# Performance work log

Hardware: AMD Instinct MI355X
Metric: run time of the kernel (lower is better)

Reference implementation:

```python
import jax, jax.numpy as jnp
import numpy as np

DIM = 3
N = DIM * DIM          # 9 digits
NUM_NODES = N * N      # 81 cells
HID = 96
EMB = 16

def sudoku_edges():
    edges = []
    for r in range(N):
        for c in range(N):
            s = set()
            for k in range(N):
                s.add(r * N + k)
                s.add(k * N + c)
            br, bc = (r // DIM) * DIM, (c // DIM) * DIM
            for dr in range(DIM):
                for dc in range(DIM):
                    s.add((br + dr) * N + (bc + dc))
            s.discard(r * N + c)
            edges.append(sorted(s))
    return np.asarray(edges, np.int32)  # (81, 20)

EDGES = jnp.asarray(sudoku_edges())

def mlp(x, params):
    # ReLU between hidden layers, no activation after the last layer
    for w, b in params[:-1]:
        x = jax.nn.relu(x @ w + b)
    w, b = params[-1]
    return x @ w + b

def setup_inputs():
    key = jax.random.key(0)
    ks = iter(jax.random.split(key, 64))
    B = 256
    def p(shape, scale=0.1):
        return jax.random.normal(next(ks), shape, jnp.float32) * scale
    inp = {}
    inp['grids'] = jax.random.randint(next(ks), (B, NUM_NODES), 0, 3)
    inp['iters'] = 8
    inp['emb'] = p((3, EMB))
    inp['in_w0'] = p((EMB, HID)); inp['in_b0'] = jnp.zeros((HID,), jnp.float32)
    inp['in_w1'] = p((HID, HID)); inp['in_b1'] = jnp.zeros((HID,), jnp.float32)
    inp['in_w2'] = p((HID, HID)); inp['in_b2'] = jnp.zeros((HID,), jnp.float32)
    inp['rel_w0'] = p((2 * HID, HID)); inp['rel_b0'] = jnp.zeros((HID,), jnp.float32)
    inp['rel_w1'] = p((HID, HID)); inp['rel_b1'] = jnp.zeros((HID,), jnp.float32)
    inp['rel_w2'] = p((HID, HID)); inp['rel_b2'] = jnp.zeros((HID,), jnp.float32)
    inp['g_w0'] = p((2 * HID, HID)); inp['g_b0'] = jnp.zeros((HID,), jnp.float32)
    inp['g_w1'] = p((HID, HID)); inp['g_b1'] = jnp.zeros((HID,), jnp.float32)
    inp['g_w2'] = p((HID, HID)); inp['g_b2'] = jnp.zeros((HID,), jnp.float32)
    inp['lstm_wih'] = p((HID, 4 * HID)); inp['lstm_whh'] = p((HID, 4 * HID))
    inp['lstm_bih'] = jnp.zeros((4 * HID,), jnp.float32)
    inp['lstm_bhh'] = jnp.zeros((4 * HID,), jnp.float32)
    inp['r_w0'] = p((HID, HID)); inp['r_b0'] = jnp.zeros((HID,), jnp.float32)
    inp['r_w1'] = p((HID, HID)); inp['r_b1'] = jnp.zeros((HID,), jnp.float32)
    inp['r_w2'] = p((HID, N)); inp['r_b2'] = jnp.zeros((N,), jnp.float32)
    inp['c0'] = p((B * NUM_NODES, HID), 1.0)  # torch.randn LSTM cell init
    return inp

def reference(grids, iters, emb, in_w0, in_b0, in_w1, in_b1, in_w2, in_b2,
              rel_w0, rel_b0, rel_w1, rel_b1, rel_w2, rel_b2,
              g_w0, g_b0, g_w1, g_b1, g_w2, g_b2,
              lstm_wih, lstm_whh, lstm_bih, lstm_bhh,
              r_w0, r_b0, r_w1, r_b1, r_w2, r_b2, c0):
    B = grids.shape[0]
    in_p = [(in_w0, in_b0), (in_w1, in_b1), (in_w2, in_b2)]
    rel_p = [(rel_w0, rel_b0), (rel_w1, rel_b1), (rel_w2, rel_b2)]
    g_p = [(g_w0, g_b0), (g_w1, g_b1), (g_w2, g_b2)]
    r_p = [(r_w0, r_b0), (r_w1, r_b1), (r_w2, r_b2)]
    X = mlp(emb[grids], in_p)                     # (B, 81, 96)
    H0 = jax.lax.stop_gradient(X)                 # X.clone().detach()
    h = H0.reshape(B * NUM_NODES, HID)
    bias = lstm_bih + lstm_bhh

    def step(carry, _):
        h, c = carry
        Hn = h.reshape(B, NUM_NODES, HID)
        nbr = Hn[:, EDGES]                        # (B, 81, 20, 96) neighbor gather
        self_f = jnp.broadcast_to(Hn[:, :, None], nbr.shape)
        msgs = mlp(jnp.concatenate([self_f, nbr], axis=-1), rel_p)
        M = msgs.sum(axis=2)                      # scatter-sum of messages
        x_in = mlp(jnp.concatenate([X, M], axis=-1), g_p).reshape(B * NUM_NODES, HID)
        gates = x_in @ lstm_wih + h @ lstm_whh + bias
        i, f, g, o = jnp.split(gates, 4, axis=-1)  # torch gate order i,f,g,o
        c2 = jax.nn.sigmoid(f) * c + jax.nn.sigmoid(i) * jnp.tanh(g)
        h2 = jax.nn.sigmoid(o) * jnp.tanh(c2)
        out = mlp(h2.reshape(B, NUM_NODES, HID), r_p)  # (B, 81, 9)
        return (h2, c2), out

    _, outputs = jax.lax.scan(step, (h, c0), None, length=iters)
    return outputs  # (iters, B, 81, 9)
```

## Files before the change

kernel.cpp:

```cpp
#include <hip/hip_runtime.h>
#include <hip/hip_bf16.h>
#include <stdint.h>

typedef __attribute__((ext_vector_type(8))) short short8v;
typedef __attribute__((ext_vector_type(4))) float float4v;

#define DEVI __device__ __forceinline__

constexpr int BATCH = 256;
constexpr int NN   = 81;
constexpr int HID  = 96;
constexpr int NOUT = 9;
constexpr int BLOCK = 512;
constexpr int LDA = 100;

constexpr int OFF_H  = 0;
constexpr int OFF_AP = 8100;
constexpr int OFF_BV = 16200;
constexpr int OFF_MS = 24300;
constexpr int OFF_XG = 32400;
constexpr int SMEM_F = 40176;

constexpr int W_REL0A = 0;
constexpr int W_REL0B = 18432;
constexpr int W_REL1  = 36864;
constexpr int W_REL2  = 55296;
constexpr int W_G0B   = 73728;
constexpr int W_G1    = 92160;
constexpr int W_G2    = 110592;
constexpr int W_IH    = 129024;
constexpr int W_HH    = 202752;
constexpr int W_R0    = 276480;
constexpr int W_R1    = 294912;
constexpr int W_R2    = 313344;
constexpr int W_IN1   = 316416;
constexpr int W_IN2   = 334848;
constexpr int W_G0A   = 353280;

DEVI float sigm(float x)  { return 1.f / (1.f + __expf(-x)); }
DEVI float tanh_(float x) { return 1.f - 2.f / (__expf(2.f * x) + 1.f); }

DEVI short bfhi(float x) { union { float f; unsigned u; } v; v.f = x; return (short)(v.u >> 16); }
DEVI float fromBits(short s) { union { unsigned u; float f; } v; v.u = ((unsigned)(unsigned short)s) << 16; return v.f; }
DEVI short bfrne(float x) {
  union { float f; unsigned u; } v; v.f = x;
  unsigned r = v.u + 0x7fffu + ((v.u >> 16) & 1u);
  return (short)(r >> 16);
}
DEVI void split1(float x, short& h, short& l) { h = bfhi(x); l = bfrne(x - fromBits(h)); }

DEVI void packFrag(const float* p, short8v& v) {
  const float4 a = *reinterpret_cast<const float4*>(p);
  const float4 b = *reinterpret_cast<const float4*>(p + 4);
  v[0] = bfrne(a.x); v[1] = bfrne(a.y); v[2] = bfrne(a.z); v[3] = bfrne(a.w);
  v[4] = bfrne(b.x); v[5] = bfrne(b.y); v[6] = bfrne(b.z); v[7] = bfrne(b.w);
}
DEVI void packFragPair(const float* ap, const float* bp, short8v& v) {
  const float4 a0 = *reinterpret_cast<const float4*>(ap);
  const float4 a1 = *reinterpret_cast<const float4*>(ap + 4);
  const float4 b0 = *reinterpret_cast<const float4*>(bp);
  const float4 b1 = *reinterpret_cast<const float4*>(bp + 4);
  v[0] = bfrne(fmaxf(a0.x + b0.x, 0.f)); v[1] = bfrne(fmaxf(a0.y + b0.y, 0.f));
  v[2] = bfrne(fmaxf(a0.z + b0.z, 0.f)); v[3] = bfrne(fmaxf(a0.w + b0.w, 0.f));
  v[4] = bfrne(fmaxf(a1.x + b1.x, 0.f)); v[5] = bfrne(fmaxf(a1.y + b1.y, 0.f));
  v[6] = bfrne(fmaxf(a1.z + b1.z, 0.f)); v[7] = bfrne(fmaxf(a1.w + b1.w, 0.f));
}

DEVI float4v mfma2(short8v a, short8v bh, short8v bl, float4v acc) {
  acc = __builtin_amdgcn_mfma_f32_16x16x32_bf16(a, bh, acc, 0, 0, 0);
  acc = __builtin_amdgcn_mfma_f32_16x16x32_bf16(a, bl, acc, 0, 0, 0);
  return acc;
}

DEVI int nbr_of(int n, int e) {
  const int r = n / 9, c = n - 9 * r;
  if (e < 8)  { int cc = c + 1 + e;  if (cc >= 9) cc -= 9; return r * 9 + cc; }
  if (e < 16) { int rr = r + e - 7;  if (rr >= 9) rr -= 9; return rr * 9 + c; }
  const int q = e - 16, dr = 1 + (q >> 1), dc = 1 + (q & 1);
  const int rm = r % 3, cm = c % 3;
  int rr = r - rm + rm + dr; rr -= (rm + dr >= 3) ? 3 : 0;
  int cc = c - cm + cm + dc; cc -= (cm + dc >= 3) ? 3 : 0;
  return rr * 9 + cc;
}

__global__ __launch_bounds__(64)
void pack_kernel(const float* rel_w0, const float* rel_w1, const float* rel_w2,
                 const float* g_w0, const float* g_w1, const float* g_w2,
                 const float* wih, const float* whh,
                 const float* r_w0, const float* r_w1, const float* r_w2,
                 const float* in_w1, const float* in_w2, short* ws)
{
  const int lane = threadIdx.x;
  const int blk = blockIdx.x;
  const int starts[16] = {0,18,36,54,72,90,108,126,198,270,288,306,309,327,345,363};
  int mi = 0;
  while (blk >= starts[mi + 1]) ++mi;
  const int tt = blk - starts[mi];
  const int ntile = starts[mi + 1] - starts[mi];
  const float* src; int C = 96, row0 = 0, off;
  switch (mi) {
    case 0:  src = rel_w0; off = W_REL0A; break;
    case 1:  src = rel_w0; row0 = 96; off = W_REL0B; break;
    case 2:  src = rel_w1; off = W_REL1; break;
    case 3:  src = rel_w2; off = W_REL2; break;
    case 4:  src = g_w0; row0 = 96; off = W_G0B; break;
    case 5:  src = g_w1; off = W_G1; break;
    case 6:  src = g_w2; off = W_G2; break;
    case 7:  src = wih; C = 384; off = W_IH; break;
    case 8:  src = whh; C = 384; off = W_HH; break;
    case 9:  src = r_w0; off = W_R0; break;
    case 10: src = r_w1; off = W_R1; break;
    case 11: src = r_w2; C = 9; off = W_R2; break;
    case 12: src = in_w1; off = W_IN1; break;
    case 13: src = in_w2; off = W_IN2; break;
    default: src = g_w0; off = W_G0A; break;
  }
  const int kt = tt % 3, ct = tt / 3;
  const int q = lane >> 4, r = lane & 15;
  const int c = ct * 16 + r;
  short* hd = ws + off + tt * 512 + lane * 8;
  short* ld = hd + ntile * 512;
  #pragma unroll
  for (int j = 0; j < 8; ++j) {
    const int k = row0 + kt * 32 + q * 8 + j;
    float w = (c < C) ? src[k * C + c] : 0.f;
    short h, l; split1(w, h, l);
    hd[j] = h; ld[j] = l;
  }
}

DEVI void stage96(float* sm, int aOff, const short* WS, int wOff, int wTiles, int CT,
                  const float* bias, float bscale, bool relu, bool xgAdd,
                  float* dst, int dstLD, int wave, int lane)
{
  const int rl = lane & 15, q = lane >> 4;
  const int plane = wTiles * 512;
  #pragma unroll 1
  for (int t = wave; t < 3 * CT; t += 8) {
    const int rtp = t % 3, ct = t / 3;
    short8v a2[2][3];
    #pragma unroll
    for (int sub = 0; sub < 2; ++sub) {
      const int row = rtp * 32 + sub * 16 + rl;
      const float* ap = &sm[aOff + row * LDA + q * 8];
      #pragma unroll
      for (int kt = 0; kt < 3; ++kt) packFrag(ap + kt * 32, a2[sub][kt]);
    }
    float4v acc0 = {0.f, 0.f, 0.f, 0.f}, acc1 = {0.f, 0.f, 0.f, 0.f};
    #pragma unroll
    for (int kt = 0; kt < 3; ++kt) {
      const short* bp = WS + wOff + (ct * 3 + kt) * 512 + lane * 8;
      const short8v bh = *reinterpret_cast<const short8v*>(bp);
      const short8v bl = *reinterpret_cast<const short8v*>(bp + plane);
      acc0 = mfma2(a2[0][kt], bh, bl, acc0);
      acc1 = mfma2(a2[1][kt], bh, bl, acc1);
    }
    const int col = ct * 16 + rl;
    #pragma unroll
    for (int sub = 0; sub < 2; ++sub) {
      #pragma unroll
      for (int j = 0; j < 4; ++j) {
        const int row = rtp * 32 + sub * 16 + q * 4 + j;
        if (row < NN) {
          float v = sub ? acc1[j] : acc0[j];
          if (bias)  v += bias[col] * bscale;
          if (xgAdd) v += sm[OFF_XG + row * 96 + col];
          if (relu)  v = fmaxf(v, 0.f);
          dst[row * dstLD + col] = v;
        }
      }
    }
  }
}

__global__ __launch_bounds__(BLOCK) __attribute__((amdgpu_waves_per_eu(1, 2)))
void rrn_kernel(const int* __restrict__ grids, const int* __restrict__ itersp,
                const float* __restrict__ emb, const float* __restrict__ in_w0,
                const float* __restrict__ in_b0, const float* __restrict__ in_b1,
                const float* __restrict__ in_b2,
                const float* __restrict__ rel_b0, const float* __restrict__ rel_b1,
                const float* __restrict__ rel_b2,
                const float* __restrict__ g_b0, const float* __restrict__ g_b1,
                const float* __restrict__ g_b2,
                const float* __restrict__ bih, const float* __restrict__ bhh,
                const float* __restrict__ r_b0, const float* __restrict__ r_b1,
                const float* __restrict__ r_b2,
                const float* __restrict__ c0, const short* __restrict__ WS,
                float* __restrict__ out)
{
  __shared__ float sm[SMEM_F];
  const int b = blockIdx.x, tid = threadIdx.x;
  const int wave = tid >> 6, lane = tid & 63;
  const int rl = lane & 15, q = lane >> 4;
  const int iters = itersp[0];

  float creg[6][4];
  #pragma unroll
  for (int rt = 0; rt < 6; ++rt)
    #pragma unroll
    for (int j = 0; j < 4; ++j) creg[rt][j] = 0.f;
  if (wave < 6) {
    #pragma unroll
    for (int rt = 0; rt < 6; ++rt) {
      #pragma unroll
      for (int j = 0; j < 4; ++j) {
        const int n = rt * 16 + q * 4 + j, col = wave * 16 + rl;
        creg[rt][j] = (n < NN) ? c0[(size_t)b * NN * HID + n * HID + col] : 0.f;
      }
    }
  }

  for (int t = tid; t < NN * HID; t += BLOCK) {
    const int n = t / HID, col = t - n * HID;
    const int g = grids[b * NN + n];
    float acc = in_b0[col];
    #pragma unroll
    for (int k = 0; k < 16; ++k) acc += emb[g * 16 + k] * in_w0[k * HID + col];
    sm[OFF_AP + n * LDA + col] = fmaxf(acc, 0.f);
  }
  __syncthreads();
  stage96(sm, OFF_AP, WS, W_IN1, 18, 6, in_b1, 1.f, true,  false, &sm[OFF_BV], LDA, wave, lane);
  __syncthreads();
  stage96(sm, OFF_BV, WS, W_IN2, 18, 6, in_b2, 1.f, false, false, &sm[OFF_H],  LDA, wave, lane);
  __syncthreads();
  stage96(sm, OFF_H,  WS, W_G0A, 18, 6, g_b0,  1.f, false, false, &sm[OFF_XG], 96,  wave, lane);
  __syncthreads();

  for (int it = 0; it < iters; ++it) {
    for (int i = tid; i < 8100; i += BLOCK) sm[OFF_MS + i] = 0.f;
    stage96(sm, OFF_H, WS, W_REL0A, 18, 6, rel_b0, 1.f, false, false, &sm[OFF_AP], LDA, wave, lane);
    stage96(sm, OFF_H, WS, W_REL0B, 18, 6, nullptr, 0.f, false, false, &sm[OFF_BV], LDA, wave, lane);
    __syncthreads();

    #pragma unroll 1
    for (int g2 = wave; g2 < 51; g2 += 8) {
      short8v a2[2][3];
      #pragma unroll
      for (int sub = 0; sub < 2; ++sub) {
        const int row = g2 * 32 + sub * 16 + rl;
        if (row < 1620) {
          const int n = row / 20, e = row - 20 * n, m = nbr_of(n, e);
          const float* ap = &sm[OFF_AP + n * LDA + q * 8];
          const float* bp = &sm[OFF_BV + m * LDA + q * 8];
          #pragma unroll
          for (int kt = 0; kt < 3; ++kt)
            packFragPair(ap + kt * 32, bp + kt * 32, a2[sub][kt]);
        } else {
          const short8v z = {0,0,0,0,0,0,0,0};
          #pragma unroll
          for (int kt = 0; kt < 3; ++kt) a2[sub][kt] = z;
        }
      }
      #pragma unroll 1
      for (int ct = 0; ct < 6; ++ct) {
        const float rb1c = rel_b1[ct * 16 + rl];
        float4v acc0 = {0,0,0,0}, acc1 = {0,0,0,0};
        #pragma unroll
        for (int kt = 0; kt < 3; ++kt) {
          const short* bp = WS + W_REL1 + (ct * 3 + kt) * 512 + lane * 8;
          const short8v bh = *reinterpret_cast<const short8v*>(bp);
          const short8v bl = *reinterpret_cast<const short8v*>(bp + 18 * 512);
          acc0 = mfma2(a2[0][kt], bh, bl, acc0);
          acc1 = mfma2(a2[1][kt], bh, bl, acc1);
        }
        const int col = ct * 16 + rl;
        #pragma unroll
        for (int sub = 0; sub < 2; ++sub) {
          const int r0 = g2 * 32 + sub * 16 + q * 4;
          if (r0 < 1620) {
            const int node = r0 / 20;
            const float4v a = sub ? acc1 : acc0;
            const float s = fmaxf(a[0] + rb1c, 0.f) + fmaxf(a[1] + rb1c, 0.f)
                          + fmaxf(a[2] + rb1c, 0.f) + fmaxf(a[3] + rb1c, 0.f);
            atomicAdd(&sm[OFF_MS + node * LDA + col], s);
          }
        }
        __builtin_amdgcn_sched_barrier(0);
      }
    }
    __syncthreads();

    stage96(sm, OFF_MS, WS, W_REL2, 18, 6, rel_b2, 20.f, false, false, &sm[OFF_AP], LDA, wave, lane);
    __syncthreads();
    stage96(sm, OFF_AP, WS, W_G0B, 18, 6, nullptr, 0.f, true, true,  &sm[OFF_BV], LDA, wave, lane);
    __syncthreads();
    stage96(sm, OFF_BV, WS, W_G1, 18, 6, g_b1, 1.f, true,  false, &sm[OFF_AP], LDA, wave, lane);
    __syncthreads();
    stage96(sm, OFF_AP, WS, W_G2, 18, 6, g_b2, 1.f, false, false, &sm[OFF_BV], LDA, wave, lane);
    __syncthreads();

    if (wave < 6) {
      const int colh = wave * 16 + rl;
      #pragma unroll
      for (int rt = 0; rt < 6; ++rt) {
        const int row = rt * 16 + rl;
        short8v af[6];
        #pragma unroll
        for (int kt = 0; kt < 3; ++kt)
          packFrag(&sm[OFF_BV + row * LDA + kt * 32 + q * 8], af[kt]);
        #pragma unroll
        for (int kt = 3; kt < 6; ++kt)
          packFrag(&sm[OFF_H + row * LDA + (kt - 3) * 32 + q * 8], af[kt]);
        float4v ga[4];
        #pragma unroll
        for (int gate = 0; gate < 4; ++gate) {
          const int ct = gate * 6 + wave;
          float4v acc = {0.f, 0.f, 0.f, 0.f};
          #pragma unroll
          for (int kt = 0; kt < 3; ++kt) {
            const short* bp = WS + W_IH + (ct * 3 + kt) * 512 + lane * 8;
            acc = mfma2(af[kt], *reinterpret_cast<const short8v*>(bp),
                        *reinterpret_cast<const short8v*>(bp + 72 * 512), acc);
          }
          __builtin_amdgcn_sched_barrier(0);
          #pragma unroll
          for (int kt = 3; kt < 6; ++kt) {
            const short* bp = WS + W_HH + (ct * 3 + kt - 3) * 512 + lane * 8;
            acc = mfma2(af[kt], *reinterpret_cast<const short8v*>(bp),
                        *reinterpret_cast<const short8v*>(bp + 72 * 512), acc);
          }
          ga[gate] = acc;
          __builtin_amdgcn_sched_barrier(0);
        }
        #pragma unroll
        for (int j = 0; j < 4; ++j) {
          const int n = rt * 16 + q * 4 + j;
          const float gi = ga[0][j] + bih[colh]       + bhh[colh];
          const float gf = ga[1][j] + bih[96 + colh]  + bhh[96 + colh];
          const float gg = ga[2][j] + bih[192 + colh] + bhh[192 + colh];
          const float go = ga[3][j] + bih[288 + colh] + bhh[288 + colh];
          const float c2 = sigm(gf) * creg[rt][j] + sigm(gi) * tanh_(gg);
          creg[rt][j] = c2;
          if (n < NN) sm[OFF_AP + n * LDA + colh] = sigm(go) * tanh_(c2);
        }
      }
    }
    __syncthreads();
    for (int i = tid; i < 8100; i += BLOCK) sm[OFF_H + i] = sm[OFF_AP + i];
    __syncthreads();

    stage96(sm, OFF_H,  WS, W_R0, 18, 6, r_b0, 1.f, true, false, &sm[OFF_AP], LDA, wave, lane);
    __syncthreads();
    stage96(sm, OFF_AP, WS, W_R1, 18, 6, r_b1, 1.f, true, false, &sm[OFF_BV], LDA, wave, lane);
    __syncthreads();
    if (wave < 3) {
      const int rtp = wave;
      short8v a2[2][3];
      #pragma unroll
      for (int sub = 0; sub < 2; ++sub) {
        const int row = rtp * 32 + sub * 16 + rl;
        #pragma unroll
        for (int kt = 0; kt < 3; ++kt)
          packFrag(&sm[OFF_BV + row * LDA + kt * 32 + q * 8], a2[sub][kt]);
      }
      float4v a0 = {0,0,0,0}, a1 = {0,0,0,0};
      #pragma unroll
      for (int kt = 0; kt < 3; ++kt) {
        const short* bp = WS + W_R2 + kt * 512 + lane * 8;
        const short8v bh = *reinterpret_cast<const short8v*>(bp);
        const short8v bl = *reinterpret_cast<const short8v*>(bp + 3 * 512);
        a0 = mfma2(a2[0][kt], bh, bl, a0);
        a1 = mfma2(a2[1][kt], bh, bl, a1);
      }
      if (rl < NOUT) {
        float* op = out + ((size_t)it * BATCH + b) * NN * NOUT;
        #pragma unroll
        for (int sub = 0; sub < 2; ++sub)
          #pragma unroll
          for (int j = 0; j < 4; ++j) {
            const int row = rtp * 32 + sub * 16 + q * 4 + j;
            if (row < NN) op[row * NOUT + rl] = (sub ? a1[j] : a0[j]) + r_b2[rl];
          }
      }
    }
    __syncthreads();
  }
}

extern "C" void kernel_launch(void* const* d_in, const int* in_sizes, int n_in,
                              void* d_out, int out_size, void* d_ws, size_t ws_size,
                              hipStream_t stream) {
  (void)in_sizes; (void)n_in; (void)out_size; (void)ws_size;
  const int* grids = (const int*)d_in[0];
  const int* iters = (const int*)d_in[1];
  const float *emb = (const float*)d_in[2],
    *in_w0 = (const float*)d_in[3],  *in_b0 = (const float*)d_in[4],
    *in_b1 = (const float*)d_in[6],  *in_b2 = (const float*)d_in[8],
    *rel_w0 = (const float*)d_in[9],  *rel_b0 = (const float*)d_in[10],
    *rel_w1 = (const float*)d_in[11], *rel_b1 = (const float*)d_in[12],
    *rel_w2 = (const float*)d_in[13], *rel_b2 = (const float*)d_in[14],
    *g_w0 = (const float*)d_in[15], *g_b0 = (const float*)d_in[16],
    *g_w1 = (const float*)d_in[17], *g_b1 = (const float*)d_in[18],
    *g_w2 = (const float*)d_in[19], *g_b2 = (const float*)d_in[20],
    *wih = (const float*)d_in[21], *whh = (const float*)d_in[22],
    *bih = (const float*)d_in[23], *bhh = (const float*)d_in[24],
    *r_w0 = (const float*)d_in[25], *r_b0 = (const float*)d_in[26],
    *r_w1 = (const float*)d_in[27], *r_b1 = (const float*)d_in[28],
    *r_w2 = (const float*)d_in[29], *r_b2 = (const float*)d_in[30],
    *c0 = (const float*)d_in[31];
  short* ws = (short*)d_ws;
  pack_kernel<<<dim3(363), dim3(64), 0, stream>>>(
      rel_w0, rel_w1, rel_w2, g_w0, g_w1, g_w2, wih, whh,
      r_w0, r_w1, r_w2, (const float*)d_in[5], (const float*)d_in[7], ws);
  rrn_kernel<<<dim3(BATCH), dim3(BLOCK), 0, stream>>>(
      grids, iters, emb, in_w0, in_b0, in_b1, in_b2,
      rel_b0, rel_b1, rel_b2, g_b0, g_b1, g_b2,
      bih, bhh, r_b0, r_b1, r_b2, c0, (const short*)ws, (float*)d_out);
}
```

Measured before the change: 919.7 us.

## Store intermediate activations as bf16 in LDS and double-buffer hidden state

The dense MLP stages now read and write their intermediate activations as bf16 in shared memory with padded stride 104. MFMA A-fragments become a single vector load instead of an fp32 read followed by packing. The hidden state is ping-ponged between two bf16 buffers, which removes the per-iteration copy loop and one barrier. This cuts LDS traffic and conversion work per stage. In exchange, more intermediates are rounded to bf16 before storage, which may slightly change numerics.

```diff
diff --git a/kernel.cpp b/kernel.cpp
--- a/kernel.cpp
+++ b/kernel.cpp
@@ -13,13 +13,15 @@
 constexpr int NOUT = 9;
 constexpr int BLOCK = 512;
 constexpr int LDA = 100;
-
-constexpr int OFF_H  = 0;
-constexpr int OFF_AP = 8100;
-constexpr int OFF_BV = 16200;
-constexpr int OFF_MS = 24300;
-constexpr int OFF_XG = 32400;
-constexpr int SMEM_F = 40176;
+constexpr int LDB = 104;
+
+constexpr int OFF_XG = 0;
+constexpr int OFF_H0 = 7776;
+constexpr int OFF_H1 = 11988;
+constexpr int OFF_MS = 16200;
+constexpr int OFF_AP = 24300;
+constexpr int OFF_BV = 32400;
+constexpr int SMEM_F = 40500;
 
 constexpr int W_REL0A = 0;
 constexpr int W_REL0B = 18432;
@@ -129,22 +131,33 @@
   }
 }
 
-DEVI void stage96(float* sm, int aOff, const short* WS, int wOff, int wTiles, int CT,
-                  const float* bias, float bscale, bool relu, bool xgAdd,
-                  float* dst, int dstLD, int wave, int lane)
+template<bool ABF, bool OBF, bool RELU, bool XGADD>
+DEVI void stage96(float* sm, int aOff, const short* WS, int wOff, int wTiles,
+                  const float* bias, float bscale, int dOff, int dstLDf,
+                  int wave, int lane)
 {
   const int rl = lane & 15, q = lane >> 4;
   const int plane = wTiles * 512;
+  const short* asb = reinterpret_cast<const short*>(sm + aOff);
+  short* dsb = reinterpret_cast<short*>(sm + dOff);
+  float* dsf = sm + dOff;
   #pragma unroll 1
-  for (int t = wave; t < 3 * CT; t += 8) {
+  for (int t = wave; t < 18; t += 8) {
     const int rtp = t % 3, ct = t / 3;
     short8v a2[2][3];
     #pragma unroll
     for (int sub = 0; sub < 2; ++sub) {
       const int row = rtp * 32 + sub * 16 + rl;
-      const float* ap = &sm[aOff + row * LDA + q * 8];
-      #pragma unroll
-      for (int kt = 0; kt < 3; ++kt) packFrag(ap + kt * 32, a2[sub][kt]);
+      if (ABF) {
+        const short* ap = asb + row * LDB + q * 8;
+        #pragma unroll
+        for (int kt = 0; kt < 3; ++kt)
+          a2[sub][kt] = *reinterpret_cast<const short8v*>(ap + kt * 32);
+      } else {
+        const float* ap = &sm[aOff + row * LDA + q * 8];
+        #pragma unroll
+        for (int kt = 0; kt < 3; ++kt) packFrag(ap + kt * 32, a2[sub][kt]);
+      }
     }
     float4v acc0 = {0.f, 0.f, 0.f, 0.f}, acc1 = {0.f, 0.f, 0.f, 0.f};
     #pragma unroll
@@ -164,9 +177,10 @@
         if (row < NN) {
           float v = sub ? acc1[j] : acc0[j];
           if (bias)  v += bias[col] * bscale;
-          if (xgAdd) v += sm[OFF_XG + row * 96 + col];
-          if (relu)  v = fmaxf(v, 0.f);
-          dst[row * dstLD + col] = v;
+          if (XGADD) v += sm[OFF_XG + row * 96 + col];
+          if (RELU)  v = fmaxf(v, 0.f);
+          if (OBF) dsb[row * LDB + col] = bfrne(v);
+          else     dsf[row * dstLDf + col] = v;
         }
       }
     }
@@ -219,17 +233,20 @@
     sm[OFF_AP + n * LDA + col] = fmaxf(acc, 0.f);
   }
   __syncthreads();
-  stage96(sm, OFF_AP, WS, W_IN1, 18, 6, in_b1, 1.f, true,  false, &sm[OFF_BV], LDA, wave, lane);
+  stage96<false, true, true,  false>(sm, OFF_AP, WS, W_IN1, 18, in_b1, 1.f, OFF_MS, 0, wave, lane);
   __syncthreads();
-  stage96(sm, OFF_BV, WS, W_IN2, 18, 6, in_b2, 1.f, false, false, &sm[OFF_H],  LDA, wave, lane);
+  stage96<true,  true, false, false>(sm, OFF_MS, WS, W_IN2, 18, in_b2, 1.f, OFF_H0, 0, wave, lane);
   __syncthreads();
-  stage96(sm, OFF_H,  WS, W_G0A, 18, 6, g_b0,  1.f, false, false, &sm[OFF_XG], 96,  wave, lane);
+  stage96<true, false, false, false>(sm, OFF_H0, WS, W_G0A, 18, g_b0,  1.f, OFF_XG, 96, wave, lane);
   __syncthreads();
 
   for (int it = 0; it < iters; ++it) {
+    const int hc = (it & 1) ? OFF_H1 : OFF_H0;
+    const int hn = (it & 1) ? OFF_H0 : OFF_H1;
+
     for (int i = tid; i < 8100; i += BLOCK) sm[OFF_MS + i] = 0.f;
-    stage96(sm, OFF_H, WS, W_REL0A, 18, 6, rel_b0, 1.f, false, false, &sm[OFF_AP], LDA, wave, lane);
-    stage96(sm, OFF_H, WS, W_REL0B, 18, 6, nullptr, 0.f, false, false, &sm[OFF_BV], LDA, wave, lane);
+    stage96<true, false, false, false>(sm, hc, WS, W_REL0A, 18, rel_b0, 1.f, OFF_AP, LDA, wave, lane);
+    stage96<true, false, false, false>(sm, hc, WS, W_REL0B, 18, nullptr, 0.f, OFF_BV, LDA, wave, lane);
     __syncthreads();
 
     #pragma unroll 1
@@ -280,27 +297,30 @@
     }
     __syncthreads();
 
-    stage96(sm, OFF_MS, WS, W_REL2, 18, 6, rel_b2, 20.f, false, false, &sm[OFF_AP], LDA, wave, lane);
-    __syncthreads();
-    stage96(sm, OFF_AP, WS, W_G0B, 18, 6, nullptr, 0.f, true, true,  &sm[OFF_BV], LDA, wave, lane);
-    __syncthreads();
-    stage96(sm, OFF_BV, WS, W_G1, 18, 6, g_b1, 1.f, true,  false, &sm[OFF_AP], LDA, wave, lane);
-    __syncthreads();
-    stage96(sm, OFF_AP, WS, W_G2, 18, 6, g_b2, 1.f, false, false, &sm[OFF_BV], LDA, wave, lane);
+    stage96<false, true, false, false>(sm, OFF_MS, WS, W_REL2, 18, rel_b2, 20.f, OFF_AP, 0, wave, lane);
+    __syncthreads();
+    stage96<true, true, true, true >(sm, OFF_AP, WS, W_G0B, 18, nullptr, 0.f, OFF_MS, 0, wave, lane);
+    __syncthreads();
+    stage96<true, true, true, false>(sm, OFF_MS, WS, W_G1, 18, g_b1, 1.f, OFF_AP, 0, wave, lane);
+    __syncthreads();
+    stage96<true, true, false, false>(sm, OFF_AP, WS, W_G2, 18, g_b2, 1.f, OFF_MS, 0, wave, lane);
     __syncthreads();
 
     if (wave < 6) {
       const int colh = wave * 16 + rl;
+      const short* xs = reinterpret_cast<const short*>(sm + OFF_MS);
+      const short* hs = reinterpret_cast<const short*>(sm + hc);
+      short* hnp = reinterpret_cast<short*>(sm + hn);
       #pragma unroll
       for (int rt = 0; rt < 6; ++rt) {
         const int row = rt * 16 + rl;
         short8v af[6];
         #pragma unroll
         for (int kt = 0; kt < 3; ++kt)
-          packFrag(&sm[OFF_BV + row * LDA + kt * 32 + q * 8], af[kt]);
+          af[kt] = *reinterpret_cast<const short8v*>(xs + row * LDB + kt * 32 + q * 8);
         #pragma unroll
         for (int kt = 3; kt < 6; ++kt)
-          packFrag(&sm[OFF_H + row * LDA + (kt - 3) * 32 + q * 8], af[kt]);
+          af[kt] = *reinterpret_cast<const short8v*>(hs + row * LDB + (kt - 3) * 32 + q * 8);
         float4v ga[4];
         #pragma unroll
         for (int gate = 0; gate < 4; ++gate) {
@@ -331,27 +351,26 @@
           const float go = ga[3][j] + bih[288 + colh] + bhh[288 + colh];
           const float c2 = sigm(gf) * creg[rt][j] + sigm(gi) * tanh_(gg);
           creg[rt][j] = c2;
-          if (n < NN) sm[OFF_AP + n * LDA + colh] = sigm(go) * tanh_(c2);
-        }
-      }
-    }
-    __syncthreads();
-    for (int i = tid; i < 8100; i += BLOCK) sm[OFF_H + i] = sm[OFF_AP + i];
-    __syncthreads();
-
-    stage96(sm, OFF_H,  WS, W_R0, 18, 6, r_b0, 1.f, true, false, &sm[OFF_AP], LDA, wave, lane);
-    __syncthreads();
-    stage96(sm, OFF_AP, WS, W_R1, 18, 6, r_b1, 1.f, true, false, &sm[OFF_BV], LDA, wave, lane);
+          if (n < NN) hnp[n * LDB + colh] = bfrne(sigm(go) * tanh_(c2));
+        }
+      }
+    }
+    __syncthreads();
+
+    stage96<true, true, true, false>(sm, hn, WS, W_R0, 18, r_b0, 1.f, OFF_AP, 0, wave, lane);
+    __syncthreads();
+    stage96<true, true, true, false>(sm, OFF_AP, WS, W_R1, 18, r_b1, 1.f, OFF_MS, 0, wave, lane);
     __syncthreads();
     if (wave < 3) {
       const int rtp = wave;
+      const short* asb = reinterpret_cast<const short*>(sm + OFF_MS);
       short8v a2[2][3];
       #pragma unroll
       for (int sub = 0; sub < 2; ++sub) {
         const int row = rtp * 32 + sub * 16 + rl;
         #pragma unroll
         for (int kt = 0; kt < 3; ++kt)
-          packFrag(&sm[OFF_BV + row * LDA + kt * 32 + q * 8], a2[sub][kt]);
+          a2[sub][kt] = *reinterpret_cast<const short8v*>(asb + row * LDB + kt * 32 + q * 8);
       }
       float4v a0 = {0,0,0,0}, a1 = {0,0,0,0};
       #pragma unroll
```

Measured after the change: 823.4 us. -10.5%, faster.
